# Kernel tuning notes

Hardware: AMD Instinct MI355X
Metric: run time of the kernel (lower is better)

The kernel has to match this reference:

```python
import jax, jax.numpy as jnp
import numpy as np

DECAY = 1.0
T_SCALE = 100.0


def setup_inputs() -> dict:
    key = jax.random.key(0)
    k1, k2, k3, k4, k5, k6 = jax.random.split(key, 6)
    S, K, N = 8192, 50, 100
    times = jnp.sort(jax.random.uniform(k1, (S,), dtype=jnp.float32) * T_SCALE)
    events = jax.random.randint(k2, (S,), 0, K, dtype=jnp.int32)
    devices = jax.random.randint(k3, (S,), 0, N, dtype=jnp.int32)
    # raw (pre-softplus) parameters, matching torch init scales
    mu_raw = jax.random.uniform(k4, (K,), dtype=jnp.float32) * 0.1
    alpha_raw = jax.random.uniform(k5, (K, K), dtype=jnp.float32) * 0.1
    adj_raw = jnp.eye(N, dtype=jnp.float32) + 0.1
    return {"times": times, "events": events, "devices": devices,
            "mu_raw": mu_raw, "alpha_raw": alpha_raw, "adj_raw": adj_raw}


def reference(times, events, devices, mu_raw, alpha_raw, adj_raw):
    mu = jax.nn.softplus(mu_raw)
    alpha = jax.nn.softplus(alpha_raw)
    adj = jax.nn.softplus(adj_raw)

    S = times.shape[0]
    # strictly-causal mask: contribution of event j < i
    mask = jnp.tril(jnp.ones((S, S), dtype=bool), -1)
    dt = times[:, None] - times[None, :]                      # [S,S], t_i - t_j
    dt_safe = jnp.where(mask, dt, 0.0)
    kernel = jnp.where(mask, jnp.exp(-DECAY * dt_safe), 0.0)  # exp decay, causal
    topo = adj[devices][:, devices]                           # [i,j] = adj[u_i, u_j]
    event_eff = alpha[events][:, events].T                    # [i,j] = alpha[e_j, e_i]
    excitation = jnp.sum(topo * event_eff * kernel, axis=1)   # [S]

    intensity = mu[events] + excitation
    log_lambda_sum = jnp.sum(jnp.log(intensity + 1e-6))

    T_end = times[-1]
    term1 = mu.sum() * T_end
    time_integral = (1.0 / DECAY) * (1.0 - jnp.exp(-DECAY * (T_end - times)))
    sum_alpha = alpha.sum(axis=1)[events]                     # sum_k alpha[e_j, k]
    sum_adj = adj.sum(axis=0)[devices]                        # sum_v adj[v, u_j]
    term2 = jnp.sum(sum_adj * sum_alpha * time_integral)

    loss = -(log_lambda_sum - (term1 + term2))
    return loss
```

## Files before the change

### kernel.cpp

```cpp
#include <hip/hip_runtime.h>
#include <math.h>


#define BLK 256
#define TI 8
#define NMAX 128
#define KMAX 64
#define MAXSPAN 1792

static_assert(TI == BLK / 32, "group-sum code assumes 8 groups of 32 lanes");

__device__ __forceinline__ float sp(float x) { return log1pf(expf(x)); }

__global__ __launch_bounds__(BLK) void main_k(
    const float* __restrict__ times, const int* __restrict__ events,
    const int* __restrict__ devices, int S, int K, int N,
    const float* __restrict__ mu_raw, const float* __restrict__ alpha_raw,
    const float* __restrict__ adj_raw, float2* __restrict__ partials)
{
    __shared__ float s_adj[TI][NMAX];
    __shared__ float s_alp[TI][KMAX];
    __shared__ float s_ti[TI];
    __shared__ int   s_ei[TI], s_ui[TI];
    __shared__ float s_mu[TI];
    __shared__ float s_sa[TI];
    __shared__ float s_sl[TI];
    __shared__ float s_red[BLK / 64][TI];
    __shared__ float s_fin[2 * TI];

    int tid   = threadIdx.x;
    int ibase = blockIdx.x * TI;

    if (tid < TI) {
        int i = ibase + tid;
        int ic = (i < S) ? i : (S - 1);
        s_ti[tid] = times[ic];
        s_ei[tid] = events[ic];
        s_ui[tid] = devices[ic];
    }
    __syncthreads();

    for (int idx = tid; idx < TI * N; idx += BLK) {
        int ii = idx / N, v = idx - ii * N;
        s_adj[ii][v] = sp(adj_raw[s_ui[ii] * N + v]);
    }
    for (int idx = tid; idx < TI * K; idx += BLK) {
        int ii = idx / K, k = idx - ii * K;
        s_alp[ii][k] = sp(alpha_raw[k * K + s_ei[ii]]);
    }

    {
        int g = tid >> 5, l = tid & 31;
        int u = s_ui[g], e = s_ei[g];
        float sa = 0.f, sl = 0.f;
        for (int r = l; r < N; r += 32) sa += sp(adj_raw[r * N + u]);
        for (int k = l; k < K; k += 32) sl += sp(alpha_raw[e * K + k]);
#pragma unroll
        for (int off = 16; off; off >>= 1) {
            sa += __shfl_xor(sa, off, 64);
            sl += __shfl_xor(sl, off, 64);
        }
        if (l == 0) { s_sa[g] = sa; s_sl[g] = sl; }
    }
    if (tid < TI) s_mu[tid] = sp(mu_raw[s_ei[tid]]);

    float t0 = s_ti[0];

    int jstart = (ibase > MAXSPAN) ? ((ibase - MAXSPAN) & ~(BLK - 1)) : 0;
    __syncthreads();

    float acc[TI];
#pragma unroll
    for (int ii = 0; ii < TI; ++ii) acc[ii] = 0.f;

    int imax = (ibase + TI <= S) ? (ibase + TI) : S;
    int jend = imax - 1;

    for (int jb = jstart; jb < jend; jb += BLK) {
        int j = jb + tid;
        bool inb = (j < jend);
        float e0 = 0.f;
        int ej = 0, uj = 0;
        if (inb) {
            float tj = times[j]; ej = events[j]; uj = devices[j];
            e0 = expf(tj - t0);
        }
        if (jb + BLK <= ibase) {
#pragma unroll
            for (int ii = 0; ii < TI; ++ii)
                acc[ii] = fmaf(s_adj[ii][uj] * s_alp[ii][ej], e0, acc[ii]);
        } else if (inb) {
#pragma unroll
            for (int ii = 0; ii < TI; ++ii) {
                float c = s_adj[ii][uj] * s_alp[ii][ej] * e0;
                acc[ii] += (j < ibase + ii) ? c : 0.f;
            }
        }
    }

#pragma unroll
    for (int ii = 0; ii < TI; ++ii) {
        float v = acc[ii];
        for (int off = 32; off; off >>= 1) v += __shfl_xor(v, off, 64);
        if ((tid & 63) == 0) s_red[tid >> 6][ii] = v;
    }
    __syncthreads();

    if (tid < TI) {
        int ii = tid;
        float lg = 0.f, t2 = 0.f;
        if (ibase + ii < S) {
            float tot = s_red[0][ii] + s_red[1][ii] + s_red[2][ii] + s_red[3][ii];
            float scale = expf(t0 - s_ti[ii]);
            float exc = tot * scale;
            float inten = s_mu[ii] + exc;
            lg = logf(inten + 1e-6f);
            float T_end = times[S - 1];
            float integ = 1.0f - expf(s_ti[ii] - T_end);
            t2 = s_sa[ii] * s_sl[ii] * integ;
        }
        s_fin[ii] = lg;
        s_fin[TI + ii] = t2;
    }
    __syncthreads();
    if (tid == 0) {
        float lg = 0.f, t2 = 0.f;
#pragma unroll
        for (int ii = 0; ii < TI; ++ii) { lg += s_fin[ii]; t2 += s_fin[TI + ii]; }
        partials[blockIdx.x] = make_float2(lg, t2);
    }
}

__global__ __launch_bounds__(BLK) void fin_k(
    const float2* __restrict__ partials, int nblocks,
    const float* __restrict__ mu_raw, int K,
    const float* __restrict__ times, int S,
    float* __restrict__ out)
{
    int tid = threadIdx.x;
    double lg = 0.0, t2 = 0.0, ms = 0.0;
    for (int b = tid; b < nblocks; b += BLK) {
        float2 p = partials[b];
        lg += (double)p.x;
        t2 += (double)p.y;
    }
    for (int k = tid; k < K; k += BLK) ms += (double)sp(mu_raw[k]);
    for (int off = 32; off; off >>= 1) {
        lg += __shfl_xor(lg, off, 64);
        t2 += __shfl_xor(t2, off, 64);
        ms += __shfl_xor(ms, off, 64);
    }
    __shared__ double s_lg[BLK / 64], s_t2[BLK / 64], s_ms[BLK / 64];
    if ((tid & 63) == 0) { s_lg[tid >> 6] = lg; s_t2[tid >> 6] = t2; s_ms[tid >> 6] = ms; }
    __syncthreads();
    if (tid == 0) {
        double L = 0.0, T2 = 0.0, M = 0.0;
        for (int w = 0; w < BLK / 64; ++w) { L += s_lg[w]; T2 += s_t2[w]; M += s_ms[w]; }
        double T_end = (double)times[S - 1];
        double term1 = M * T_end;
        double loss = -(L - (term1 + T2));
        out[0] = (float)loss;
    }
}

extern "C" void kernel_launch(void* const* d_in, const int* in_sizes, int n_in,
                              void* d_out, int out_size, void* d_ws, size_t ws_size,
                              hipStream_t stream)
{
    const float* times     = (const float*)d_in[0];
    const int*   events    = (const int*)d_in[1];
    const int*   devices   = (const int*)d_in[2];
    const float* mu_raw    = (const float*)d_in[3];
    const float* alpha_raw = (const float*)d_in[4];
    const float* adj_raw   = (const float*)d_in[5];

    int S = in_sizes[0];
    int K = in_sizes[3];
    int NN = in_sizes[5];
    int N = 1;
    while (N * N < NN) ++N;

    float2* partials = (float2*)d_ws;
    int nblocks = (S + TI - 1) / TI;

    main_k<<<nblocks, BLK, 0, stream>>>(times, events, devices, S, K, N,
                                        mu_raw, alpha_raw, adj_raw, partials);
    fin_k<<<1, BLK, 0, stream>>>(partials, nblocks, mu_raw, K, times, S, (float*)d_out);
}
```

Baseline: 84.60 us.

## Precompute softplus tables and row sums in a prep kernel; use fast exp/log

Adds a prep kernel that applies softplus once to mu, alpha (stored transposed), and adj, and precomputes the per-event alpha row sums and per-device adj column sums. The main kernel's 1024 blocks then copy their rows from these tables instead of each recomputing many softplus values with expf/log1pf on every launch. The main loop and epilogue also switch to __expf/__logf intrinsics. This costs an extra kernel launch and a workspace round trip, and the fast intrinsics are slightly less accurate.

Result: faster. 79.32 us (-6.2%).

```diff
diff --git a/kernel.cpp b/kernel.cpp
--- a/kernel.cpp
+++ b/kernel.cpp
@@ -8,23 +8,58 @@
 #define KMAX 64
 #define MAXSPAN 1792
 
-static_assert(TI == BLK / 32, "group-sum code assumes 8 groups of 32 lanes");
-
 __device__ __forceinline__ float sp(float x) { return log1pf(expf(x)); }
+
+__global__ __launch_bounds__(BLK) void prep_k(
+    const float* __restrict__ mu_raw, const float* __restrict__ alpha_raw,
+    const float* __restrict__ adj_raw, int K, int N,
+    float* __restrict__ mu_sp, float* __restrict__ alpha_spT,
+    float* __restrict__ adj_sp, float* __restrict__ sum_alpha,
+    float* __restrict__ sum_adj)
+{
+    int b = blockIdx.x, tid = threadIdx.x;
+    if (b < K) {
+        for (int k = tid; k < K; k += BLK)
+            alpha_spT[b * K + k] = sp(alpha_raw[k * K + b]);
+    } else if (b < K + N) {
+        int r = b - K;
+        for (int v = tid; v < N; v += BLK)
+            adj_sp[r * N + v] = sp(adj_raw[r * N + v]);
+    } else if (b == K + N) {
+        for (int k = tid; k < K; k += BLK)
+            mu_sp[k] = sp(mu_raw[k]);
+    } else if (b <= 2 * K + N) {
+        if (tid < 64) {
+            int e = b - (K + N + 1);
+            float s = (tid < K) ? sp(alpha_raw[e * K + tid]) : 0.f;
+#pragma unroll
+            for (int off = 32; off; off >>= 1) s += __shfl_xor(s, off, 64);
+            if (tid == 0) sum_alpha[e] = s;
+        }
+    } else {
+        if (tid < 64) {
+            int v = b - (2 * K + N + 1);
+            float s = (tid < N) ? sp(adj_raw[tid * N + v]) : 0.f;
+            if (tid + 64 < N) s += sp(adj_raw[(tid + 64) * N + v]);
+#pragma unroll
+            for (int off = 32; off; off >>= 1) s += __shfl_xor(s, off, 64);
+            if (tid == 0) sum_adj[v] = s;
+        }
+    }
+}
 
 __global__ __launch_bounds__(BLK) void main_k(
     const float* __restrict__ times, const int* __restrict__ events,
     const int* __restrict__ devices, int S, int K, int N,
-    const float* __restrict__ mu_raw, const float* __restrict__ alpha_raw,
-    const float* __restrict__ adj_raw, float2* __restrict__ partials)
+    const float* __restrict__ mu_sp, const float* __restrict__ alpha_spT,
+    const float* __restrict__ adj_sp, const float* __restrict__ sum_alpha,
+    const float* __restrict__ sum_adj, float2* __restrict__ partials)
 {
     __shared__ float s_adj[TI][NMAX];
     __shared__ float s_alp[TI][KMAX];
     __shared__ float s_ti[TI];
     __shared__ int   s_ei[TI], s_ui[TI];
-    __shared__ float s_mu[TI];
-    __shared__ float s_sa[TI];
-    __shared__ float s_sl[TI];
+    __shared__ float s_mu[TI], s_sa[TI], s_sl[TI];
     __shared__ float s_red[BLK / 64][TI];
     __shared__ float s_fin[2 * TI];
 
@@ -40,32 +75,23 @@
     }
     __syncthreads();
 
-    for (int idx = tid; idx < TI * N; idx += BLK) {
-        int ii = idx / N, v = idx - ii * N;
-        s_adj[ii][v] = sp(adj_raw[s_ui[ii] * N + v]);
-    }
-    for (int idx = tid; idx < TI * K; idx += BLK) {
-        int ii = idx / K, k = idx - ii * K;
-        s_alp[ii][k] = sp(alpha_raw[k * K + s_ei[ii]]);
-    }
-
-    {
-        int g = tid >> 5, l = tid & 31;
-        int u = s_ui[g], e = s_ei[g];
-        float sa = 0.f, sl = 0.f;
-        for (int r = l; r < N; r += 32) sa += sp(adj_raw[r * N + u]);
-        for (int k = l; k < K; k += 32) sl += sp(alpha_raw[e * K + k]);
-#pragma unroll
-        for (int off = 16; off; off >>= 1) {
-            sa += __shfl_xor(sa, off, 64);
-            sl += __shfl_xor(sl, off, 64);
-        }
-        if (l == 0) { s_sa[g] = sa; s_sl[g] = sl; }
-    }
-    if (tid < TI) s_mu[tid] = sp(mu_raw[s_ei[tid]]);
+#pragma unroll
+    for (int ii = 0; ii < TI; ++ii) {
+        int u = s_ui[ii];
+        for (int v = tid; v < N; v += BLK) s_adj[ii][v] = adj_sp[u * N + v];
+    }
+#pragma unroll
+    for (int ii = 0; ii < TI; ++ii) {
+        int e = s_ei[ii];
+        for (int k = tid; k < K; k += BLK) s_alp[ii][k] = alpha_spT[e * K + k];
+    }
+    if (tid < TI) {
+        s_mu[tid] = mu_sp[s_ei[tid]];
+        s_sl[tid] = sum_alpha[s_ei[tid]];
+        s_sa[tid] = sum_adj[s_ui[tid]];
+    }
 
     float t0 = s_ti[0];
-
     int jstart = (ibase > MAXSPAN) ? ((ibase - MAXSPAN) & ~(BLK - 1)) : 0;
     __syncthreads();
 
@@ -83,7 +109,7 @@
         int ej = 0, uj = 0;
         if (inb) {
             float tj = times[j]; ej = events[j]; uj = devices[j];
-            e0 = expf(tj - t0);
+            e0 = __expf(tj - t0);
         }
         if (jb + BLK <= ibase) {
 #pragma unroll
@@ -111,12 +137,12 @@
         float lg = 0.f, t2 = 0.f;
         if (ibase + ii < S) {
             float tot = s_red[0][ii] + s_red[1][ii] + s_red[2][ii] + s_red[3][ii];
-            float scale = expf(t0 - s_ti[ii]);
+            float scale = __expf(t0 - s_ti[ii]);
             float exc = tot * scale;
             float inten = s_mu[ii] + exc;
-            lg = logf(inten + 1e-6f);
+            lg = __logf(inten + 1e-6f);
             float T_end = times[S - 1];
-            float integ = 1.0f - expf(s_ti[ii] - T_end);
+            float integ = 1.0f - __expf(s_ti[ii] - T_end);
             t2 = s_sa[ii] * s_sl[ii] * integ;
         }
         s_fin[ii] = lg;
@@ -180,10 +206,24 @@
     int N = 1;
     while (N * N < NN) ++N;
 
-    float2* partials = (float2*)d_ws;
+    float* ws = (float*)d_ws;
+    float* mu_sp     = ws;
+    float* alpha_spT = mu_sp + K;
+    float* adj_sp    = alpha_spT + K * K;
+    float* sum_alpha = adj_sp + N * N;
+    float* sum_adj   = sum_alpha + K;
+    float* endp      = sum_adj + N;
+    size_t off = (size_t)(endp - ws);
+    off = (off + 1) & ~(size_t)1;
+    float2* partials = (float2*)(ws + off);
+
     int nblocks = (S + TI - 1) / TI;
-
+    int pblocks = 2 * K + 2 * N + 1;
+
+    prep_k<<<pblocks, BLK, 0, stream>>>(mu_raw, alpha_raw, adj_raw, K, N,
+                                        mu_sp, alpha_spT, adj_sp, sum_alpha, sum_adj);
     main_k<<<nblocks, BLK, 0, stream>>>(times, events, devices, S, K, N,
-                                        mu_raw, alpha_raw, adj_raw, partials);
+                                        mu_sp, alpha_spT, adj_sp, sum_alpha, sum_adj,
+                                        partials);
     fin_k<<<1, BLK, 0, stream>>>(partials, nblocks, mu_raw, K, times, S, (float*)d_out);
 }
```
